# Optimization experiments

Measured on AMD Instinct MI355X. Metric: run time of the kernel, lower is better.

The kernel has to match this reference:

```python
import jax, jax.numpy as jnp
import numpy as np

N = 16384      # num nodes
F_IN = 128     # in_features
F_OUT = 128    # out_features


def setup_inputs() -> dict:
    key = jax.random.key(0)
    k1, k2, k3 = jax.random.split(key, 3)
    inp = jax.random.normal(k1, (N, F_IN), dtype=jnp.float32)
    adj = jax.random.uniform(k2, (N, N), dtype=jnp.float32)
    stdv = 1.0 / np.sqrt(F_OUT)
    weight = jax.random.uniform(k3, (F_IN * 2, F_OUT), dtype=jnp.float32,
                                minval=-stdv, maxval=stdv)
    return {"input": inp, "adj": adj, "weight": weight}


def reference(input, adj, weight):
    # support = adj @ input  (dense aggregation, [N, F])
    support = jnp.matmul(adj, input)
    # concat [input, support] -> [N, 2F], then transform -> [N, out]
    # Avoid materializing the concat by splitting the weight matmul:
    w_self, w_agg = weight[:F_IN], weight[F_IN:]
    return jnp.matmul(input, w_self) + jnp.matmul(support, w_agg)
```

## Files before the change

### kernel.cpp

```cpp
#include <hip/hip_runtime.h>


#define NROWS 16384
#define FDIM  128
#define NT2   128

typedef __attribute__((ext_vector_type(4))) float f32x4;
typedef __attribute__((ext_vector_type(8))) short short8;
typedef __attribute__((ext_vector_type(8))) __bf16 bf16x8;
typedef __attribute__((ext_vector_type(8))) unsigned short ushort8;

static __device__ __forceinline__ unsigned short f2bf(float f) {
  union { __bf16 b; unsigned short u; } cvt;
  cvt.b = (__bf16)f;
  return cvt.u;
}

__global__ __launch_bounds__(256, 2)
void gcn_prep(const float* __restrict__ input, const float* __restrict__ weight,
              unsigned short* __restrict__ Yt, float* __restrict__ Z)
{
  __shared__ __align__(16) float in_lds[32 * FDIM];
  const int tid = threadIdx.x;
  const int m0  = blockIdx.x * 32;

  const f32x4* src = (const f32x4*)(input + (size_t)m0 * FDIM);
  f32x4* dst = (f32x4*)in_lds;
#pragma unroll
  for (int i = 0; i < 4; ++i) dst[i * 256 + tid] = src[i * 256 + tid];
  __syncthreads();

  const int c  = tid & 127;
  const int rg = tid >> 7;

  float accz[16], accy[16];
#pragma unroll
  for (int r = 0; r < 16; ++r) { accz[r] = 0.f; accy[r] = 0.f; }

  for (int k4 = 0; k4 < 32; ++k4) {
    float wsv[4], wav[4];
#pragma unroll
    for (int j = 0; j < 4; ++j) {
      wsv[j] = weight[(size_t)(k4 * 4 + j) * FDIM + c];
      wav[j] = weight[(size_t)(k4 * 4 + j + FDIM) * FDIM + c];
    }
#pragma unroll
    for (int r = 0; r < 16; ++r) {
      const f32x4 vin = *(const f32x4*)&in_lds[(rg * 16 + r) * FDIM + k4 * 4];
#pragma unroll
      for (int j = 0; j < 4; ++j) {
        accz[r] += vin[j] * wsv[j];
        accy[r] += vin[j] * wav[j];
      }
    }
  }

#pragma unroll
  for (int r = 0; r < 16; ++r)
    Z[(size_t)(m0 + rg * 16 + r) * FDIM + c] = accz[r];

  const int kt = m0 >> 7;
#pragma unroll
  for (int g = 0; g < 2; ++g) {
    const int mbase = m0 + rg * 16 + g * 8;
    const int ch = (mbase >> 3) & 15;
    ushort8 v;
#pragma unroll
    for (int j = 0; j < 8; ++j) v[j] = f2bf(accy[g * 8 + j]);
    *(ushort8*)&Yt[(size_t)kt * 16384 + (size_t)(ch * 128 + c) * 8] = v;
  }
}

__global__ __launch_bounds__(512, 1)
void gcn_main(const float* __restrict__ adj, const unsigned short* __restrict__ Yt,
              const float* __restrict__ Z, float* __restrict__ out)
{
  __shared__ __align__(16) unsigned char lds[2][65536];

  const int tid  = threadIdx.x;
  const int lane = tid & 63;
  const int wv   = tid >> 6;
  const int rg   = wv >> 1;
  const int nh   = wv & 1;
  const int m0   = blockIdx.x * 64;
  const int rlo  = lane & 15;
  const int kgrp = lane >> 4;

  f32x4 acc[4];
#pragma unroll
  for (int f = 0; f < 4; ++f) acc[f] = (f32x4){0.f, 0.f, 0.f, 0.f};

  auto stage = [&](int buf, int kt) {
    const unsigned short* bs = Yt + (size_t)kt * 16384;
#pragma unroll
    for (int i = 0; i < 4; ++i) {
      const int q = wv * 4 + i;
      __builtin_amdgcn_global_load_lds(
          (const __attribute__((address_space(1))) void*)(bs + q * 512 + lane * 8),
          (__attribute__((address_space(3))) void*)(&lds[buf][q * 1024]),
          16, 0, 0);
    }
#pragma unroll
    for (int i = 0; i < 4; ++i) {
      const int p     = wv * 4 + i;
      const int row_g = 2 * p + (lane >> 5);
      const int j     = (lane & 31) ^ (row_g & 7);
      const float* as = adj + (size_t)(m0 + row_g) * NROWS + (size_t)kt * 128 + j * 4;
      __builtin_amdgcn_global_load_lds(
          (const __attribute__((address_space(1))) void*)as,
          (__attribute__((address_space(3))) void*)(&lds[buf][32768 + p * 1024]),
          16, 0, 2 );
    }
  };

  stage(0, 0);
  stage(1, 1);

  const int arow = (rg * 16 + rlo) * 512;
  const int aswz = rlo & 7;

  for (int kt = 0; kt < NT2; ++kt) {
    if (kt < NT2 - 1) {
      asm volatile("s_waitcnt vmcnt(8)" ::: "memory");
    } else {
      asm volatile("s_waitcnt vmcnt(0)" ::: "memory");
    }
    __builtin_amdgcn_sched_barrier(0);
    __builtin_amdgcn_s_barrier();
    __builtin_amdgcn_sched_barrier(0);

    const int buf = kt & 1;
    const unsigned char* Bp = lds[buf];
    const unsigned char* Ap = Bp + 32768;

    short8 a8[4];
#pragma unroll
    for (int s = 0; s < 4; ++s) {
      const int c0 = s * 8 + kgrp * 2;
      const f32x4 lo = *(const f32x4*)(Ap + arow + ((c0    ) ^ aswz) * 16);
      const f32x4 hi = *(const f32x4*)(Ap + arow + ((c0 + 1) ^ aswz) * 16);
      bf16x8 av;
#pragma unroll
      for (int j = 0; j < 4; ++j) {
        av[j]     = (__bf16)lo[j];
        av[j + 4] = (__bf16)hi[j];
      }
      a8[s] = __builtin_bit_cast(short8, av);
    }

#pragma unroll
    for (int s = 0; s < 4; ++s) {
      const int ch = s * 4 + kgrp;
#pragma unroll
      for (int f = 0; f < 4; ++f) {
        const int n = nh * 64 + f * 16 + rlo;
        const short8 b8 = *(const short8*)(Bp + (size_t)(ch * 128 + n) * 16);
        acc[f] = __builtin_amdgcn_mfma_f32_16x16x32_bf16(a8[s], b8, acc[f], 0, 0, 0);
      }
    }

    __builtin_amdgcn_s_barrier();
    __builtin_amdgcn_sched_barrier(0);
    if (kt + 2 < NT2) stage(buf, kt + 2);
  }

  const int rowb = m0 + rg * 16 + (lane >> 4) * 4;
#pragma unroll
  for (int f = 0; f < 4; ++f) {
    const int col = nh * 64 + f * 16 + rlo;
#pragma unroll
    for (int r = 0; r < 4; ++r) {
      const size_t idx = (size_t)(rowb + r) * FDIM + col;
      out[idx] = acc[f][r] + Z[idx];
    }
  }
}

extern "C" void kernel_launch(void* const* d_in, const int* in_sizes, int n_in,
                              void* d_out, int out_size, void* d_ws, size_t ws_size,
                              hipStream_t stream) {
  const float* input  = (const float*)d_in[0];
  const float* adj    = (const float*)d_in[1];
  const float* weight = (const float*)d_in[2];
  float* out = (float*)d_out;

  unsigned short* Yt = (unsigned short*)d_ws;
  float* Z = (float*)((char*)d_ws + (size_t)NROWS * FDIM * 2);

  gcn_prep<<<512, 256, 0, stream>>>(input, weight, Yt, Z);
  gcn_main<<<256, 512, 0, stream>>>(adj, Yt, Z, out);
}
```

Measured before the change: 206.9 us.

## Load B operand straight into registers and double the adj K-tile per stage

The main kernel stops staging the bf16 Yt tiles through LDS. Each wave now loads its B fragments straight into registers with inline global_load_dwordx4, double-buffered in two register arrays. The adj tile per LDS stage grows to 256 columns, which halves the number of stages and barriers, and hand-tuned vmcnt waits overlap the B loads with MFMA work. This frees LDS bandwidth and cuts synchronization, at the cost of more VGPRs and fragile manual wait counts. The kernel is probably bounded by streaming adj from memory, so the gain may be small.

```diff
diff --git a/kernel.cpp b/kernel.cpp
--- a/kernel.cpp
+++ b/kernel.cpp
@@ -3,7 +3,7 @@
 
 #define NROWS 16384
 #define FDIM  128
-#define NT2   128
+#define NTI   64
 
 typedef __attribute__((ext_vector_type(4))) float f32x4;
 typedef __attribute__((ext_vector_type(8))) short short8;
@@ -71,11 +71,57 @@
   }
 }
 
+
+#define BLOAD(BK_, H_)                                                                        \
+  { const char* _bb = (const char*)Yt + (size_t)(H_) * 32768 + boff;                          \
+    const char* _b0 = _bb;                                                                    \
+    const char* _b1 = _bb + 8192;                                                             \
+    const char* _b2 = _bb + 16384;                                                            \
+    const char* _b3 = _bb + 24576;                                                            \
+    asm volatile("global_load_dwordx4 %0, %1, off"            : "=v"(BK_[ 0]) : "v"(_b0));    \
+    asm volatile("global_load_dwordx4 %0, %1, off offset:256" : "=v"(BK_[ 1]) : "v"(_b0));    \
+    asm volatile("global_load_dwordx4 %0, %1, off offset:512" : "=v"(BK_[ 2]) : "v"(_b0));    \
+    asm volatile("global_load_dwordx4 %0, %1, off offset:768" : "=v"(BK_[ 3]) : "v"(_b0));    \
+    asm volatile("global_load_dwordx4 %0, %1, off"            : "=v"(BK_[ 4]) : "v"(_b1));    \
+    asm volatile("global_load_dwordx4 %0, %1, off offset:256" : "=v"(BK_[ 5]) : "v"(_b1));    \
+    asm volatile("global_load_dwordx4 %0, %1, off offset:512" : "=v"(BK_[ 6]) : "v"(_b1));    \
+    asm volatile("global_load_dwordx4 %0, %1, off offset:768" : "=v"(BK_[ 7]) : "v"(_b1));    \
+    asm volatile("global_load_dwordx4 %0, %1, off"            : "=v"(BK_[ 8]) : "v"(_b2));    \
+    asm volatile("global_load_dwordx4 %0, %1, off offset:256" : "=v"(BK_[ 9]) : "v"(_b2));    \
+    asm volatile("global_load_dwordx4 %0, %1, off offset:512" : "=v"(BK_[10]) : "v"(_b2));    \
+    asm volatile("global_load_dwordx4 %0, %1, off offset:768" : "=v"(BK_[11]) : "v"(_b2));    \
+    asm volatile("global_load_dwordx4 %0, %1, off"            : "=v"(BK_[12]) : "v"(_b3));    \
+    asm volatile("global_load_dwordx4 %0, %1, off offset:256" : "=v"(BK_[13]) : "v"(_b3));    \
+    asm volatile("global_load_dwordx4 %0, %1, off offset:512" : "=v"(BK_[14]) : "v"(_b3));    \
+    asm volatile("global_load_dwordx4 %0, %1, off offset:768" : "=v"(BK_[15]) : "v"(_b3));    \
+  }
+
+#define CHALF(Ap_, H_, BK_)                                                                   \
+  { _Pragma("unroll")                                                                         \
+    for (int _sl = 0; _sl < 4; ++_sl) {                                                       \
+      const int _c0 = ((H_) * 4 + _sl) * 8 + kgrp * 2;                                        \
+      const f32x4 _lo = *(const f32x4*)((Ap_) + arow + (((_c0    ) ^ aswz) * 16));            \
+      const f32x4 _hi = *(const f32x4*)((Ap_) + arow + (((_c0 + 1) ^ aswz) * 16));            \
+      bf16x8 _av;                                                                             \
+      _Pragma("unroll")                                                                       \
+      for (int _j = 0; _j < 4; ++_j) { _av[_j] = (__bf16)_lo[_j]; _av[_j+4] = (__bf16)_hi[_j]; } \
+      const short8 _a8 = __builtin_bit_cast(short8, _av);                                     \
+      acc[0] = __builtin_amdgcn_mfma_f32_16x16x32_bf16(_a8, BK_[_sl*4+0], acc[0], 0, 0, 0);   \
+      acc[1] = __builtin_amdgcn_mfma_f32_16x16x32_bf16(_a8, BK_[_sl*4+1], acc[1], 0, 0, 0);   \
+      acc[2] = __builtin_amdgcn_mfma_f32_16x16x32_bf16(_a8, BK_[_sl*4+2], acc[2], 0, 0, 0);   \
+      acc[3] = __builtin_amdgcn_mfma_f32_16x16x32_bf16(_a8, BK_[_sl*4+3], acc[3], 0, 0, 0);   \
+    } }
+
+#define VMCNT(n) do { asm volatile("s_waitcnt vmcnt(" #n ")" ::: "memory");                   \
+                      __builtin_amdgcn_sched_barrier(0); } while (0)
+#define BAR()    do { __builtin_amdgcn_s_barrier();                                           \
+                      __builtin_amdgcn_sched_barrier(0); } while (0)
+
 __global__ __launch_bounds__(512, 1)
 void gcn_main(const float* __restrict__ adj, const unsigned short* __restrict__ Yt,
               const float* __restrict__ Z, float* __restrict__ out)
 {
-  __shared__ __align__(16) unsigned char lds[2][65536];
+  __shared__ __align__(16) unsigned char abuf[2][65536];
 
   const int tid  = threadIdx.x;
   const int lane = tid & 63;
@@ -86,82 +132,65 @@
   const int rlo  = lane & 15;
   const int kgrp = lane >> 4;
 
+  const int arow = (rg * 16 + rlo) * 1024;
+  const int aswz = rlo & 7;
+  const int boff = kgrp * 2048 + (nh * 64 + rlo) * 16;
+
   f32x4 acc[4];
 #pragma unroll
   for (int f = 0; f < 4; ++f) acc[f] = (f32x4){0.f, 0.f, 0.f, 0.f};
 
-  auto stage = [&](int buf, int kt) {
-    const unsigned short* bs = Yt + (size_t)kt * 16384;
-#pragma unroll
-    for (int i = 0; i < 4; ++i) {
-      const int q = wv * 4 + i;
-      __builtin_amdgcn_global_load_lds(
-          (const __attribute__((address_space(1))) void*)(bs + q * 512 + lane * 8),
-          (__attribute__((address_space(3))) void*)(&lds[buf][q * 1024]),
-          16, 0, 0);
-    }
-#pragma unroll
-    for (int i = 0; i < 4; ++i) {
-      const int p     = wv * 4 + i;
-      const int row_g = 2 * p + (lane >> 5);
-      const int j     = (lane & 31) ^ (row_g & 7);
-      const float* as = adj + (size_t)(m0 + row_g) * NROWS + (size_t)kt * 128 + j * 4;
+  short8 bk0[16], bk1[16];
+
+  auto stageA = [&](int buf, int kt2) {
+#pragma unroll
+    for (int i = 0; i < 8; ++i) {
+      const int r = wv * 8 + i;
+      const int j = lane ^ (r & 7);
+      const float* as = adj + (size_t)(m0 + r) * NROWS + (size_t)kt2 * 256 + (size_t)j * 4;
       __builtin_amdgcn_global_load_lds(
           (const __attribute__((address_space(1))) void*)as,
-          (__attribute__((address_space(3))) void*)(&lds[buf][32768 + p * 1024]),
+          (__attribute__((address_space(3))) void*)(&abuf[buf][r * 1024]),
           16, 0, 2 );
     }
   };
 
-  stage(0, 0);
-  stage(1, 1);
-
-  const int arow = (rg * 16 + rlo) * 512;
-  const int aswz = rlo & 7;
-
-  for (int kt = 0; kt < NT2; ++kt) {
-    if (kt < NT2 - 1) {
-      asm volatile("s_waitcnt vmcnt(8)" ::: "memory");
-    } else {
-      asm volatile("s_waitcnt vmcnt(0)" ::: "memory");
-    }
-    __builtin_amdgcn_sched_barrier(0);
-    __builtin_amdgcn_s_barrier();
-    __builtin_amdgcn_sched_barrier(0);
-
-    const int buf = kt & 1;
-    const unsigned char* Bp = lds[buf];
-    const unsigned char* Ap = Bp + 32768;
-
-    short8 a8[4];
-#pragma unroll
-    for (int s = 0; s < 4; ++s) {
-      const int c0 = s * 8 + kgrp * 2;
-      const f32x4 lo = *(const f32x4*)(Ap + arow + ((c0    ) ^ aswz) * 16);
-      const f32x4 hi = *(const f32x4*)(Ap + arow + ((c0 + 1) ^ aswz) * 16);
-      bf16x8 av;
-#pragma unroll
-      for (int j = 0; j < 4; ++j) {
-        av[j]     = (__bf16)lo[j];
-        av[j + 4] = (__bf16)hi[j];
-      }
-      a8[s] = __builtin_bit_cast(short8, av);
-    }
-
-#pragma unroll
-    for (int s = 0; s < 4; ++s) {
-      const int ch = s * 4 + kgrp;
-#pragma unroll
-      for (int f = 0; f < 4; ++f) {
-        const int n = nh * 64 + f * 16 + rlo;
-        const short8 b8 = *(const short8*)(Bp + (size_t)(ch * 128 + n) * 16);
-        acc[f] = __builtin_amdgcn_mfma_f32_16x16x32_bf16(a8[s], b8, acc[f], 0, 0, 0);
-      }
-    }
-
-    __builtin_amdgcn_s_barrier();
-    __builtin_amdgcn_sched_barrier(0);
-    if (kt + 2 < NT2) stage(buf, kt + 2);
+  stageA(0, 0);
+  stageA(1, 1);
+  BLOAD(bk0, 0);
+
+  {
+    const unsigned char* Ap = abuf[0];
+    BLOAD(bk1, 1);
+    VMCNT(16);
+    BAR();
+    CHALF(Ap, 0, bk0);
+    BLOAD(bk0, 2);
+    VMCNT(16);
+    CHALF(Ap, 1, bk1);
+    BAR();
+    stageA(0, 2);
+  }
+
+  for (int kt = 1; kt <= NTI - 2; ++kt) {
+    const unsigned char* Ap = abuf[kt & 1];
+    BLOAD(bk1, 2 * kt + 1);
+    VMCNT(24);
+    CHALF(Ap, 0, bk0);
+    BLOAD(bk0, 2 * kt + 2);
+    VMCNT(16);
+    CHALF(Ap, 1, bk1);
+    BAR();
+    if (kt < NTI - 2) stageA(kt & 1, kt + 2);
+  }
+
+  {
+    const unsigned char* Ap = abuf[1];
+    BLOAD(bk1, 127);
+    VMCNT(16);
+    CHALF(Ap, 0, bk0);
+    VMCNT(0);
+    CHALF(Ap, 1, bk1);
   }
 
   const int rowb = m0 + rg * 16 + (lane >> 4) * 4;
```

Result: slower. 291.6 us (+40.9%).

## Use bf16 MFMA for input-weight projection in prep kernel

Applied to the files above, without the earlier changes.

Rewrites the prep kernel so the input x weight projection (Z and Y) runs on bf16 MFMA instructions instead of scalar fp32 FMAs. Input and transposed weight are converted to bf16 and stored in swizzled LDS, and each block now handles 64 rows, with the grid halved. This targets the FP32 ALU cost of the small projection GEMM, which runs before the dominant adj matmul. In exchange, the self term Z is now computed in bf16 precision, and every block reloads and transposes the full weight matrix into LDS.

```diff
diff --git a/kernel.cpp b/kernel.cpp
--- a/kernel.cpp
+++ b/kernel.cpp
@@ -8,7 +8,7 @@
 typedef __attribute__((ext_vector_type(4))) float f32x4;
 typedef __attribute__((ext_vector_type(8))) short short8;
 typedef __attribute__((ext_vector_type(8))) __bf16 bf16x8;
-typedef __attribute__((ext_vector_type(8))) unsigned short ushort8;
+typedef __attribute__((ext_vector_type(4))) unsigned short ushort4v;
 
 static __device__ __forceinline__ unsigned short f2bf(float f) {
   union { __bf16 b; unsigned short u; } cvt;
@@ -20,54 +20,79 @@
 void gcn_prep(const float* __restrict__ input, const float* __restrict__ weight,
               unsigned short* __restrict__ Yt, float* __restrict__ Z)
 {
-  __shared__ __align__(16) float in_lds[32 * FDIM];
-  const int tid = threadIdx.x;
-  const int m0  = blockIdx.x * 32;
-
-  const f32x4* src = (const f32x4*)(input + (size_t)m0 * FDIM);
-  f32x4* dst = (f32x4*)in_lds;
-#pragma unroll
-  for (int i = 0; i < 4; ++i) dst[i * 256 + tid] = src[i * 256 + tid];
+  __shared__ __align__(16) unsigned short inA[8192];
+  __shared__ __align__(16) unsigned short Wt[32768];
+  char* inA_c = (char*)inA;
+  char* Wt_c  = (char*)Wt;
+
+  const int tid  = threadIdx.x;
+  const int lane = tid & 63;
+  const int wv   = tid >> 6;
+  const int m0g  = blockIdx.x * 64;
+
+#pragma unroll
+  for (int p = 0; p < 8; ++p) {
+    const int idx4 = tid + p * 256;
+    const int row  = idx4 >> 5;
+    const int k0   = (idx4 & 31) * 4;
+    const f32x4 v  = *(const f32x4*)(input + (size_t)(m0g + row) * FDIM + k0);
+    ushort4v u;
+#pragma unroll
+    for (int i = 0; i < 4; ++i) u[i] = f2bf(v[i]);
+    *(ushort4v*)(inA_c + row * 256 + ((k0 * 2) ^ ((row & 7) << 4))) = u;
+  }
+#pragma unroll
+  for (int p = 0; p < 32; ++p) {
+    const int e4   = tid + p * 256;
+    const int krow = e4 >> 5;
+    const int n0   = (e4 & 31) * 4;
+    const f32x4 v  = *(const f32x4*)(weight + (size_t)krow * FDIM + n0);
+    const int k  = krow & 127;
+    const int nb = (krow >> 7) * 128;
+#pragma unroll
+    for (int i = 0; i < 4; ++i) {
+      const int n = nb + n0 + i;
+      *(unsigned short*)(Wt_c + n * 256 + ((k * 2) ^ ((n & 7) << 4))) = f2bf(v[i]);
+    }
+  }
   __syncthreads();
 
-  const int c  = tid & 127;
-  const int rg = tid >> 7;
-
-  float accz[16], accy[16];
-#pragma unroll
-  for (int r = 0; r < 16; ++r) { accz[r] = 0.f; accy[r] = 0.f; }
-
-  for (int k4 = 0; k4 < 32; ++k4) {
-    float wsv[4], wav[4];
-#pragma unroll
-    for (int j = 0; j < 4; ++j) {
-      wsv[j] = weight[(size_t)(k4 * 4 + j) * FDIM + c];
-      wav[j] = weight[(size_t)(k4 * 4 + j + FDIM) * FDIM + c];
-    }
-#pragma unroll
-    for (int r = 0; r < 16; ++r) {
-      const f32x4 vin = *(const f32x4*)&in_lds[(rg * 16 + r) * FDIM + k4 * 4];
-#pragma unroll
-      for (int j = 0; j < 4; ++j) {
-        accz[r] += vin[j] * wsv[j];
-        accy[r] += vin[j] * wav[j];
-      }
-    }
-  }
-
-#pragma unroll
-  for (int r = 0; r < 16; ++r)
-    Z[(size_t)(m0 + rg * 16 + r) * FDIM + c] = accz[r];
-
-  const int kt = m0 >> 7;
-#pragma unroll
-  for (int g = 0; g < 2; ++g) {
-    const int mbase = m0 + rg * 16 + g * 8;
-    const int ch = (mbase >> 3) & 15;
-    ushort8 v;
-#pragma unroll
-    for (int j = 0; j < 8; ++j) v[j] = f2bf(accy[g * 8 + j]);
-    *(ushort8*)&Yt[(size_t)kt * 16384 + (size_t)(ch * 128 + c) * 8] = v;
+  const int rlo  = lane & 15;
+  const int kgrp = lane >> 4;
+  const int arow = wv * 16 + rlo;
+
+  f32x4 acc[16];
+#pragma unroll
+  for (int f = 0; f < 16; ++f) acc[f] = (f32x4){0.f, 0.f, 0.f, 0.f};
+
+#pragma unroll
+  for (int s = 0; s < 4; ++s) {
+    const int kb = s * 64 + kgrp * 16;
+    const short8 a8 = *(const short8*)(inA_c + arow * 256 + (kb ^ ((arow & 7) << 4)));
+#pragma unroll
+    for (int f = 0; f < 16; ++f) {
+      const int n = f * 16 + rlo;
+      const short8 b8 = *(const short8*)(Wt_c + n * 256 + (kb ^ ((n & 7) << 4)));
+      acc[f] = __builtin_amdgcn_mfma_f32_16x16x32_bf16(a8, b8, acc[f], 0, 0, 0);
+    }
+  }
+
+  const int mg = m0g + wv * 16 + kgrp * 4;
+#pragma unroll
+  for (int f = 0; f < 8; ++f) {
+    const int col = f * 16 + rlo;
+#pragma unroll
+    for (int r = 0; r < 4; ++r)
+      Z[(size_t)(mg + r) * FDIM + col] = acc[f][r];
+  }
+  const int H = mg >> 7, ch = (mg >> 3) & 15, kin0 = mg & 7;
+#pragma unroll
+  for (int f = 8; f < 16; ++f) {
+    const int c = f * 16 + rlo - 128;
+    ushort4v u;
+#pragma unroll
+    for (int r = 0; r < 4; ++r) u[r] = f2bf(acc[f][r]);
+    *(ushort4v*)(Yt + (size_t)H * 16384 + (size_t)(ch * 128 + c) * 8 + kin0) = u;
   }
 }
 
@@ -187,6 +212,6 @@
   unsigned short* Yt = (unsigned short*)d_ws;
   float* Z = (float*)((char*)d_ws + (size_t)NROWS * FDIM * 2);
 
-  gcn_prep<<<512, 256, 0, stream>>>(input, weight, Yt, Z);
+  gcn_prep<<<256, 256, 0, stream>>>(input, weight, Yt, Z);
   gcn_main<<<256, 512, 0, stream>>>(adj, Yt, Z, out);
 }
```

Measured after the change: 198.1 us. -4.2%, faster.
